# Kernel optimization log

Hardware: AMD Instinct MI355X
Metric: run time of the kernel (lower is better)

Reference implementation:

```python
import jax, jax.numpy as jnp
import numpy as np
from jax.scipy.linalg import solve_triangular

OMEGA = 1.5  # params_fix['omega']
BS, N, MAXITER = 512, 256, 200
RTOL = 1e-6


def setup_inputs() -> dict:
    key = jax.random.key(0)
    k1, k2, k3 = jax.random.split(key, 3)
    # diagonally dominant A so SOR converges
    A = jax.random.normal(k1, (BS, N, N), jnp.float32) + N * jnp.eye(N, dtype=jnp.float32)
    b = jax.random.normal(k2, (BS, N), jnp.float32)
    x_sol = jnp.linalg.solve(A, b[..., None])[..., 0]
    theta = jax.random.normal(k3, (BS, N), jnp.float32)  # initial iterate x0
    rtol = jnp.full((BS,), RTOL, jnp.float32)
    return {"A": A, "b": b, "x_sol": x_sol, "theta": theta, "rtol": rtol, "maxiter": MAXITER}


def reference(A, b, x_sol, theta, rtol, maxiter):
    bs, n, _ = A.shape
    b = b.reshape(bs, n, 1)
    x0 = theta.reshape(bs, n, 1)
    xs = x_sol.reshape(bs, n, 1)

    diag = jnp.diagonal(A, axis1=1, axis2=2)          # [bs, n]
    D = jnp.eye(n, dtype=A.dtype) * diag[:, :, None]  # diag_embed
    L = jnp.tril(A, -1)
    U = jnp.triu(A, 1)

    omega = jnp.asarray(OMEGA, A.dtype)
    G1 = D + omega * L                      # lower triangular, [bs, n, n]
    G2 = omega * U + (omega - 1.0) * D
    G = solve_triangular(G1, -G2, lower=True)        # iteration matrix
    f = solve_triangular(G1, omega * b, lower=True)  # affine term

    err0 = jnp.linalg.norm(xs - x0, axis=(1, 2))     # [bs]
    xtol = jnp.linalg.norm(xs, axis=(1, 2)) * rtol   # [bs]

    def step(carry, _):
        x, err, done = carry
        # global stopping criterion: while any(err > xtol)
        done = jnp.logical_or(done, jnp.logical_not(jnp.any(err > xtol)))
        x_new = jnp.where(done, x, G @ x + f)
        err_new = jnp.where(done, err, jnp.linalg.norm(xs - x_new, axis=(1, 2)))
        hist = jnp.where(done, jnp.zeros_like(err), err_new)  # unwritten slots stay 0
        return (x_new, err_new, done), hist

    init = (x0, err0, jnp.asarray(False))
    _, hist = jax.lax.scan(step, init, None, length=maxiter)  # hist: [maxiter, bs]
    return jnp.concatenate([err0[:, None], hist.T], axis=1)   # [bs, maxiter+1]
```

## Files before the change

kernel.cpp:

```cpp
#include <hip/hip_runtime.h>
#include <math.h>

#define BS 512
#define NN 256
#define RB 16
#define OMEGA_F 1.5f

__global__ __launch_bounds__(1024)
void sor_fused(
    const float* __restrict__ A,
    const float* __restrict__ xs,
    const float* __restrict__ x0,
    const float* __restrict__ rtol,
    const int* __restrict__ maxiter_p,
    float* __restrict__ out)
{
    const int b   = blockIdx.x;
    const int tid = threadIdx.x;
    const int t   = tid & 255;
    const int q   = tid >> 8;
    const int qU  = __builtin_amdgcn_readfirstlane(q);
    const int w   = __builtin_amdgcn_readfirstlane(tid >> 6);
    const int u   = tid & 63;
    const float* __restrict__ Ab = A + (size_t)b * NN * NN;

    __shared__ __align__(16) char smem[65536];
    float (*ldsA)[NN]     = (float (*)[NN])(smem);
    float (*acc2)[RB][NN] = (float (*)[RB][NN])(smem + 16384);
    float (*xbuf)[NN]     = (float (*)[NN])(smem + 16384);
    float (*ldsX)[NN]     = (float (*)[NN])(smem);
    float* rs             = (float*)(smem + 16384);
    float* e              = (float*)(smem);
    float (*pbuf)[4][64]  = (float (*)[4][64])(smem + 1024);
    float* nrm            = (float*)(smem + 1024 + 16384);

    const int mi = *maxiter_p;
    float* __restrict__ outb = out + (size_t)b * (mi + 1);

    float ev = 0.f;
    if (q == 0) {
        const float xsv = xs[b * NN + t];
        ev = xsv - x0[b * NN + t];
        float s1 = ev * ev, s2 = xsv * xsv;
        #pragma unroll
        for (int off = 32; off > 0; off >>= 1) {
            s1 += __shfl_down(s1, off);
            s2 += __shfl_down(s2, off);
        }
        if ((t & 63) == 0) { rs[t >> 6] = s1; rs[4 + (t >> 6)] = s2; }
    }
    __syncthreads();
    const float err0 = sqrtf(rs[0] + rs[1] + rs[2] + rs[3]);
    const float xtol = sqrtf(rs[4] + rs[5] + rs[6] + rs[7]) * rtol[b];
    if (tid == 0) outb[0] = err0;

    float g[4][RB];
    for (int KB = 0; KB < NN / RB; ++KB) {
        const int r0 = KB * RB;
        __syncthreads();
        {
            const int rr = tid >> 6, c4 = (tid & 63) << 2;
            *(float4*)&ldsA[rr][c4] = *(const float4*)&Ab[(size_t)(r0 + rr) * NN + c4];
        }
        __syncthreads();

        float acc[RB];
        #pragma unroll
        for (int rr = 0; rr < RB; ++rr) acc[rr] = 0.f;
        #pragma unroll
        for (int m = 0; m < 4; ++m) {
            const int kb = 4 * m + qU;
            if (kb < KB) {
                const int j0 = kb * RB;
                #pragma unroll
                for (int jw = 0; jw < 4; ++jw) {
                    const float g0 = g[m][4 * jw + 0];
                    const float g1 = g[m][4 * jw + 1];
                    const float g2 = g[m][4 * jw + 2];
                    const float g3 = g[m][4 * jw + 3];
                    #pragma unroll
                    for (int hc = 0; hc < 4; ++hc) {
                        float4 a_[4];
                        #pragma unroll
                        for (int h = 0; h < 4; ++h)
                            a_[h] = *(const float4*)&Ab[(size_t)(r0 + 4 * hc + h) * NN + j0 + 4 * jw];
                        #pragma unroll
                        for (int h = 0; h < 4; ++h)
                            acc[4 * hc + h] += a_[h].x * g0 + a_[h].y * g1
                                             + a_[h].z * g2 + a_[h].w * g3;
                    }
                }
            }
        }
        if (q >= 1) {
            #pragma unroll
            for (int rr = 0; rr < RB; ++rr) acc2[q - 1][rr][t] = acc[rr];
        }
        __syncthreads();
        if (q == 0) {
            float s_[RB];
            #pragma unroll
            for (int rr = 0; rr < RB; ++rr)
                s_[rr] = acc[rr] + acc2[0][rr][t] + acc2[1][rr][t] + acc2[2][rr][t];
            #pragma unroll
            for (int rr = 0; rr < RB; ++rr) {
                const int r = r0 + rr;
                const float a_rt = ldsA[rr][t];
                const float brt  = (t > r) ? (-OMEGA_F) * a_rt
                                 : ((t == r) ? (1.0f - OMEGA_F) * a_rt : 0.0f);
                const float diag = ldsA[rr][r];
                const float val  = (brt - OMEGA_F * s_[rr]) / diag;
                xbuf[rr][t] = val;
                #pragma unroll
                for (int rr2 = rr + 1; rr2 < RB; ++rr2)
                    s_[rr2] += ldsA[rr2][r] * val;
            }
        }
        __syncthreads();
        #pragma unroll
        for (int m = 0; m < 4; ++m) {
            if (KB == 4 * m + q) {
                #pragma unroll
                for (int rr = 0; rr < RB; ++rr) g[m][rr] = xbuf[rr][t];
            }
        }
    }

    float4 gi[4][4];
    #pragma unroll
    for (int R = 0; R < 4; ++R) {
        __syncthreads();
        #pragma unroll
        for (int rr = 0; rr < RB; ++rr) {
            const int lr = q * RB + rr;
            ldsX[lr][(t + 4 * lr) & 255] = g[R][rr];
        }
        __syncthreads();
        #pragma unroll
        for (int jj4 = 0; jj4 < 4; ++jj4) {
            const int c = 16 * w + 4 * jj4;
            gi[R][jj4] = *(const float4*)&ldsX[u][(c + 4 * u) & 255];
        }
    }
    __syncthreads();

    if (tid < NN) e[tid] = ev;
    __syncthreads();

    const float4* __restrict__ e4 = (const float4*)e;
    float err = err0;
    int s = 1;
    for (; s <= mi; ++s) {
        if (!(err > xtol)) break;
        float a0 = 0.f, a1 = 0.f, a2 = 0.f, a3 = 0.f;
        #pragma unroll
        for (int jj4 = 0; jj4 < 4; ++jj4) {
            const float4 ev4 = e4[4 * w + jj4];
            a0 += gi[0][jj4].x*ev4.x + gi[0][jj4].y*ev4.y + gi[0][jj4].z*ev4.z + gi[0][jj4].w*ev4.w;
            a1 += gi[1][jj4].x*ev4.x + gi[1][jj4].y*ev4.y + gi[1][jj4].z*ev4.z + gi[1][jj4].w*ev4.w;
            a2 += gi[2][jj4].x*ev4.x + gi[2][jj4].y*ev4.y + gi[2][jj4].z*ev4.z + gi[2][jj4].w*ev4.w;
            a3 += gi[3][jj4].x*ev4.x + gi[3][jj4].y*ev4.y + gi[3][jj4].z*ev4.z + gi[3][jj4].w*ev4.w;
        }
        pbuf[w][0][u] = a0;
        pbuf[w][1][u] = a1;
        pbuf[w][2][u] = a2;
        pbuf[w][3][u] = a3;
        __syncthreads();
        if (tid < NN) {
            const int kk = tid >> 6, uu = tid & 63;
            float sum = 0.f;
            #pragma unroll
            for (int w2 = 0; w2 < 16; ++w2) sum += pbuf[w2][kk][uu];
            e[tid] = sum;
            float loc = sum * sum;
            #pragma unroll
            for (int off = 32; off > 0; off >>= 1) loc += __shfl_down(loc, off);
            if (uu == 0) nrm[kk] = loc;
        }
        __syncthreads();
        err = sqrtf(nrm[0] + nrm[1] + nrm[2] + nrm[3]);
        if (tid == 0) outb[s] = err;
    }
    for (int idx = s + tid; idx <= mi; idx += 1024) outb[idx] = 0.f;
}

extern "C" void kernel_launch(void* const* d_in, const int* in_sizes, int n_in,
                              void* d_out, int out_size, void* d_ws, size_t ws_size,
                              hipStream_t stream) {
    const float* A     = (const float*)d_in[0];
    const float* xs    = (const float*)d_in[2];
    const float* theta = (const float*)d_in[3];
    const float* rtol  = (const float*)d_in[4];
    const int*   mi    = (const int*)d_in[5];
    float* out = (float*)d_out;

    sor_fused<<<dim3(BS), dim3(1024), 0, stream>>>(
        A, xs, theta, rtol, mi, out);
}
```

Measured before the change: 691.9 us.

## Split SOR into column-parallel G-matrix build kernel and separate iteration kernel

Splits the fused kernel in two. The first kernel computes the iteration matrix G with twice as many blocks, each handling 128 columns, and writes it to the global workspace. The second kernel reloads G, keeping half in registers and half in LDS (128 KB), which reduces register pressure during the iteration loop. The extra global round trip of 256 MB for G, the large LDS allocation and the launch overhead are traded for more parallelism in the triangular solve phase and better occupancy.

```diff
diff --git a/kernel.cpp b/kernel.cpp
--- a/kernel.cpp
+++ b/kernel.cpp
@@ -6,60 +6,34 @@
 #define RB 16
 #define OMEGA_F 1.5f
 
-__global__ __launch_bounds__(1024)
-void sor_fused(
-    const float* __restrict__ A,
-    const float* __restrict__ xs,
-    const float* __restrict__ x0,
-    const float* __restrict__ rtol,
-    const int* __restrict__ maxiter_p,
-    float* __restrict__ out)
+
+__global__ __launch_bounds__(512)
+void sor_gmat(const float* __restrict__ A, float* __restrict__ gws)
 {
-    const int b   = blockIdx.x;
+    const int bp  = blockIdx.x;
+    const int b   = bp >> 1;
+    const int p   = bp & 1;
     const int tid = threadIdx.x;
-    const int t   = tid & 255;
-    const int q   = tid >> 8;
+    const int tc  = tid & 127;
+    const int t   = 128 * p + tc;
+    const int q   = tid >> 7;
     const int qU  = __builtin_amdgcn_readfirstlane(q);
-    const int w   = __builtin_amdgcn_readfirstlane(tid >> 6);
-    const int u   = tid & 63;
     const float* __restrict__ Ab = A + (size_t)b * NN * NN;
 
-    __shared__ __align__(16) char smem[65536];
-    float (*ldsA)[NN]     = (float (*)[NN])(smem);
-    float (*acc2)[RB][NN] = (float (*)[RB][NN])(smem + 16384);
-    float (*xbuf)[NN]     = (float (*)[NN])(smem + 16384);
-    float (*ldsX)[NN]     = (float (*)[NN])(smem);
-    float* rs             = (float*)(smem + 16384);
-    float* e              = (float*)(smem);
-    float (*pbuf)[4][64]  = (float (*)[4][64])(smem + 1024);
-    float* nrm            = (float*)(smem + 1024 + 16384);
-
-    const int mi = *maxiter_p;
-    float* __restrict__ outb = out + (size_t)b * (mi + 1);
-
-    float ev = 0.f;
-    if (q == 0) {
-        const float xsv = xs[b * NN + t];
-        ev = xsv - x0[b * NN + t];
-        float s1 = ev * ev, s2 = xsv * xsv;
-        #pragma unroll
-        for (int off = 32; off > 0; off >>= 1) {
-            s1 += __shfl_down(s1, off);
-            s2 += __shfl_down(s2, off);
-        }
-        if ((t & 63) == 0) { rs[t >> 6] = s1; rs[4 + (t >> 6)] = s2; }
-    }
-    __syncthreads();
-    const float err0 = sqrtf(rs[0] + rs[1] + rs[2] + rs[3]);
-    const float xtol = sqrtf(rs[4] + rs[5] + rs[6] + rs[7]) * rtol[b];
-    if (tid == 0) outb[0] = err0;
+    __shared__ __align__(16) char smem[73728];
+    float (*ldsA)[NN]       = (float (*)[NN])(smem);
+    float (*acc2)[RB][128]  = (float (*)[RB][128])(smem + 16384);
+    float (*xbuf)[128]      = (float (*)[128])(smem + 16384);
+    float (*ldsT)[128]      = (float (*)[128])(smem + 40960);
 
     float g[4][RB];
     for (int KB = 0; KB < NN / RB; ++KB) {
         const int r0 = KB * RB;
         __syncthreads();
-        {
-            const int rr = tid >> 6, c4 = (tid & 63) << 2;
+        #pragma unroll
+        for (int i = 0; i < 2; ++i) {
+            const int lin = tid + 512 * i;
+            const int rr = lin >> 6, c4 = (lin & 63) << 2;
             *(float4*)&ldsA[rr][c4] = *(const float4*)&Ab[(size_t)(r0 + rr) * NN + c4];
         }
         __syncthreads();
@@ -94,14 +68,14 @@
         }
         if (q >= 1) {
             #pragma unroll
-            for (int rr = 0; rr < RB; ++rr) acc2[q - 1][rr][t] = acc[rr];
+            for (int rr = 0; rr < RB; ++rr) acc2[q - 1][rr][tc] = acc[rr];
         }
         __syncthreads();
         if (q == 0) {
             float s_[RB];
             #pragma unroll
             for (int rr = 0; rr < RB; ++rr)
-                s_[rr] = acc[rr] + acc2[0][rr][t] + acc2[1][rr][t] + acc2[2][rr][t];
+                s_[rr] = acc[rr] + acc2[0][rr][tc] + acc2[1][rr][tc] + acc2[2][rr][tc];
             #pragma unroll
             for (int rr = 0; rr < RB; ++rr) {
                 const int r = r0 + rr;
@@ -110,7 +84,7 @@
                                  : ((t == r) ? (1.0f - OMEGA_F) * a_rt : 0.0f);
                 const float diag = ldsA[rr][r];
                 const float val  = (brt - OMEGA_F * s_[rr]) / diag;
-                xbuf[rr][t] = val;
+                xbuf[rr][tc] = val;
                 #pragma unroll
                 for (int rr2 = rr + 1; rr2 < RB; ++rr2)
                     s_[rr2] += ldsA[rr2][r] * val;
@@ -121,31 +95,85 @@
         for (int m = 0; m < 4; ++m) {
             if (KB == 4 * m + q) {
                 #pragma unroll
-                for (int rr = 0; rr < RB; ++rr) g[m][rr] = xbuf[rr][t];
+                for (int rr = 0; rr < RB; ++rr) g[m][rr] = xbuf[rr][tc];
             }
         }
     }
 
-    float4 gi[4][4];
+    const int u8 = tid & 63, wl = tid >> 6;
+    float* __restrict__ gb = gws + (size_t)b * (NN * NN);
     #pragma unroll
     for (int R = 0; R < 4; ++R) {
         __syncthreads();
         #pragma unroll
         for (int rr = 0; rr < RB; ++rr) {
             const int lr = q * RB + rr;
-            ldsX[lr][(t + 4 * lr) & 255] = g[R][rr];
-        }
-        __syncthreads();
-        #pragma unroll
-        for (int jj4 = 0; jj4 < 4; ++jj4) {
-            const int c = 16 * w + 4 * jj4;
-            gi[R][jj4] = *(const float4*)&ldsX[u][(c + 4 * u) & 255];
-        }
-    }
+            ldsT[lr][(tc + 4 * lr) & 127] = g[R][rr];
+        }
+        __syncthreads();
+        #pragma unroll
+        for (int k = 0; k < 4; ++k) {
+            const int cl = 16 * wl + 4 * k;
+            const float4 v = *(const float4*)&ldsT[u8][(cl + 4 * u8) & 127];
+            *(float4*)&gb[((size_t)((R * 4 + k) * 16 + 8 * p + wl)) * 256 + 4 * u8] = v;
+        }
+    }
+}
+
+__global__ __launch_bounds__(1024)
+void sor_iter(const float* __restrict__ gws,
+              const float* __restrict__ xs,
+              const float* __restrict__ x0,
+              const float* __restrict__ rtol,
+              const int* __restrict__ maxiter_p,
+              float* __restrict__ out)
+{
+    const int b   = blockIdx.x;
+    const int tid = threadIdx.x;
+    const int w   = __builtin_amdgcn_readfirstlane(tid >> 6);
+    const int u   = tid & 63;
+
+    __shared__ __align__(16) char smem[148544];
+    float* gl            = (float*)smem;
+    float* e             = (float*)(smem + 131072);
+    float (*pbuf)[4][64] = (float (*)[4][64])(smem + 132096);
+    float* nrm           = (float*)(smem + 148480);
+    float* rs            = (float*)(smem + 148496);
+
+    const int mi = *maxiter_p;
+    float* __restrict__ outb = out + (size_t)b * (mi + 1);
+    const float* __restrict__ gb = gws + (size_t)b * (NN * NN);
+
+    if (tid < NN) {
+        const float xsv = xs[b * NN + tid];
+        const float ev  = xsv - x0[b * NN + tid];
+        e[tid] = ev;
+        float s1 = ev * ev, s2 = xsv * xsv;
+        #pragma unroll
+        for (int off = 32; off > 0; off >>= 1) {
+            s1 += __shfl_down(s1, off);
+            s2 += __shfl_down(s2, off);
+        }
+        if (u == 0) { rs[tid >> 6] = s1; rs[4 + (tid >> 6)] = s2; }
+    }
+
+    float4 gi[2][4];
+    #pragma unroll
+    for (int rg = 0; rg < 2; ++rg)
+        #pragma unroll
+        for (int k = 0; k < 4; ++k)
+            gi[rg][k] = *(const float4*)&gb[(size_t)((rg * 4 + k) * 16 + w) * 256 + 4 * u];
+    #pragma unroll
+    for (int rg = 0; rg < 2; ++rg)
+        #pragma unroll
+        for (int k = 0; k < 4; ++k) {
+            const float4 v = *(const float4*)&gb[(size_t)(((rg + 2) * 4 + k) * 16 + w) * 256 + 4 * u];
+            *(float4*)&gl[((rg * 4 + k) * 16 + w) * 256 + 4 * u] = v;
+        }
     __syncthreads();
-
-    if (tid < NN) e[tid] = ev;
-    __syncthreads();
+    const float err0 = sqrtf(rs[0] + rs[1] + rs[2] + rs[3]);
+    const float xtol = sqrtf(rs[4] + rs[5] + rs[6] + rs[7]) * rtol[b];
+    if (tid == 0) outb[0] = err0;
 
     const float4* __restrict__ e4 = (const float4*)e;
     float err = err0;
@@ -154,12 +182,14 @@
         if (!(err > xtol)) break;
         float a0 = 0.f, a1 = 0.f, a2 = 0.f, a3 = 0.f;
         #pragma unroll
-        for (int jj4 = 0; jj4 < 4; ++jj4) {
-            const float4 ev4 = e4[4 * w + jj4];
-            a0 += gi[0][jj4].x*ev4.x + gi[0][jj4].y*ev4.y + gi[0][jj4].z*ev4.z + gi[0][jj4].w*ev4.w;
-            a1 += gi[1][jj4].x*ev4.x + gi[1][jj4].y*ev4.y + gi[1][jj4].z*ev4.z + gi[1][jj4].w*ev4.w;
-            a2 += gi[2][jj4].x*ev4.x + gi[2][jj4].y*ev4.y + gi[2][jj4].z*ev4.z + gi[2][jj4].w*ev4.w;
-            a3 += gi[3][jj4].x*ev4.x + gi[3][jj4].y*ev4.y + gi[3][jj4].z*ev4.z + gi[3][jj4].w*ev4.w;
+        for (int k = 0; k < 4; ++k) {
+            const float4 ev4 = e4[4 * w + k];
+            const float4 v2 = *(const float4*)&gl[(k * 16 + w) * 256 + 4 * u];
+            const float4 v3 = *(const float4*)&gl[((4 + k) * 16 + w) * 256 + 4 * u];
+            a0 += gi[0][k].x*ev4.x + gi[0][k].y*ev4.y + gi[0][k].z*ev4.z + gi[0][k].w*ev4.w;
+            a1 += gi[1][k].x*ev4.x + gi[1][k].y*ev4.y + gi[1][k].z*ev4.z + gi[1][k].w*ev4.w;
+            a2 += v2.x*ev4.x + v2.y*ev4.y + v2.z*ev4.z + v2.w*ev4.w;
+            a3 += v3.x*ev4.x + v3.y*ev4.y + v3.z*ev4.z + v3.w*ev4.w;
         }
         pbuf[w][0][u] = a0;
         pbuf[w][1][u] = a1;
@@ -193,7 +223,8 @@
     const float* rtol  = (const float*)d_in[4];
     const int*   mi    = (const int*)d_in[5];
     float* out = (float*)d_out;
-
-    sor_fused<<<dim3(BS), dim3(1024), 0, stream>>>(
-        A, xs, theta, rtol, mi, out);
+    float* gws = (float*)d_ws;
+
+    sor_gmat<<<dim3(BS * 2), dim3(512), 0, stream>>>(A, gws);
+    sor_iter<<<dim3(BS), dim3(1024), 0, stream>>>(gws, A  == A ? xs : xs, theta, rtol, mi, out);
 }
```

Measured after the change: 676.3 us. -2.3%, faster.
